# Optimization experiments

Measured on AMD Instinct MI355X. Metric: run time of the kernel, lower is better.

The kernel has to match this reference:

```python
import jax, jax.numpy as jnp
import numpy as np

B, L, D, H = 2, 2048, 2048, 16
HD = D // H          # head_dim = 128
LD = HD // 4         # latent_dim = 32


def _linear_params(key, fan_in, fan_out):
    kw, kb = jax.random.split(key)
    bound = 1.0 / np.sqrt(fan_in)
    W = jax.random.uniform(kw, (fan_in, fan_out), jnp.float32, -bound, bound)
    b = jax.random.uniform(kb, (fan_out,), jnp.float32, -bound, bound)
    return W, b


def setup_inputs() -> dict:
    key = jax.random.key(0)
    ks = jax.random.split(key, 12)
    x = jax.random.normal(ks[0], (B, L, D), jnp.float32)
    cos = jax.random.uniform(ks[1], (L, HD // 2), jnp.float32)
    sin = jax.random.uniform(ks[2], (L, HD // 2), jnp.float32)
    Wq, bq = _linear_params(ks[3], D, D)
    Wk, bk = _linear_params(ks[4], D, D)
    Wv, bv = _linear_params(ks[5], D, D)
    Wqc, bqc = _linear_params(ks[6], HD, LD)
    Wkc, bkc = _linear_params(ks[7], HD, LD)
    Wvc, bvc = _linear_params(ks[8], HD, LD)
    Wd, bd = _linear_params(ks[9], LD, HD)
    Wo, bo = _linear_params(ks[10], D, D)
    return dict(x=x, cos=cos, sin=sin, Wq=Wq, bq=bq, Wk=Wk, bk=bk, Wv=Wv, bv=bv,
                Wqc=Wqc, bqc=bqc, Wkc=Wkc, bkc=bkc, Wvc=Wvc, bvc=bvc,
                Wd=Wd, bd=bd, Wo=Wo, bo=bo)


def _apply_rope(q, k, cos, sin):
    # q, k: (B, H, L, HD); cos, sin: (L, HD//2) -> broadcast over B, H
    c = cos[None, None, :, :]
    s = sin[None, None, :, :]
    qe, qo = q[..., ::2], q[..., 1::2]
    ke, ko = k[..., ::2], k[..., 1::2]
    q_rot = jnp.stack([qe * c - qo * s, qe * s + qo * c], axis=-1).reshape(q.shape)
    k_rot = jnp.stack([ke * c - ko * s, ke * s + ko * c], axis=-1).reshape(k.shape)
    return q_rot, k_rot


def reference(x, cos, sin, Wq, bq, Wk, bk, Wv, bv,
              Wqc, bqc, Wkc, bkc, Wvc, bvc, Wd, bd, Wo, bo):
    b, l, d = x.shape
    # projections -> (B, H, L, HD)
    q = (x @ Wq + bq).reshape(b, l, H, HD).transpose(0, 2, 1, 3)
    k = (x @ Wk + bk).reshape(b, l, H, HD).transpose(0, 2, 1, 3)
    v = (x @ Wv + bv).reshape(b, l, H, HD).transpose(0, 2, 1, 3)
    q, k = _apply_rope(q, k, cos, sin)
    # low-rank compression into latent_dim
    qc = jnp.einsum('bhld,de->bhle', q, Wqc) + bqc
    kc = jnp.einsum('bhld,de->bhle', k, Wkc) + bkc
    vc = jnp.einsum('bhld,de->bhle', v, Wvc) + bvc
    scores = jnp.einsum('bhqe,bhke->bhqk', qc, kc) / np.sqrt(LD).astype(np.float32)
    causal = jnp.tril(jnp.ones((l, l), dtype=bool))  # True = keep
    scores = jnp.where(causal[None, None], scores, -jnp.inf)
    probs = jax.nn.softmax(scores, axis=-1)
    attn = jnp.einsum('bhqk,bhke->bhqe', probs, vc)
    attn = jnp.einsum('bhle,ed->bhld', attn, Wd) + bd  # decompress to HD
    attn = attn.transpose(0, 2, 1, 3).reshape(b, l, d)
    return attn @ Wo + bo
```

## Files before the change

### kernel.cpp

```cpp
#include <hip/hip_runtime.h>
#include <hip/hip_bf16.h>


#define Bsz 2
#define Lseq 2048
#define Dmod 2048
#define Hn 16
#define HDim 128
#define LDim 32

typedef __bf16 bf16x8 __attribute__((ext_vector_type(8)));
typedef float f32x4 __attribute__((ext_vector_type(4)));
typedef __hip_bfloat16 bf16;

#define GLDS16(g, l)                                                    \
  __builtin_amdgcn_global_load_lds(                                     \
      (const __attribute__((address_space(1))) unsigned int*)(g),       \
      (__attribute__((address_space(3))) unsigned int*)(l), 16, 0, 0)

#define SM_COS 0
#define SM_SIN 131072
#define SM_WC 262144
#define SM_BC 274432
#define SM_WD 274528
#define SM_BD 278624
#define SM_BO 278752
#define SM_BQKV 280800
#define SM_TOT 286944

__global__ void detect_dtype(const ushort* __restrict__ x, int* __restrict__ flag) {
  int t = threadIdx.x;
  int bad = 0;
  for (int k = 0; k < 4; ++k) {
    ushort u = x[t * 4 + k];
    int ex = (u >> 7) & 0xFF;
    if (ex >= 0xC0) bad = 1;
  }
  unsigned long long b = __ballot(bad);
  if (t == 0) *flag = (b != 0ULL) ? 1 : 0;
}

__device__ inline void conv8(const void* src, size_t so, bf16* dst, size_t dof, int f32) {
  if (f32) {
    const float* s = (const float*)src + so;
    bf16 tmp[8] __attribute__((aligned(16)));
    for (int j = 0; j < 8; ++j) tmp[j] = __float2bfloat16(s[j]);
    *(uint4*)&dst[dof] = *(uint4*)tmp;
  } else {
    *(uint4*)&dst[dof] = *(const uint4*)((const ushort*)src + so);
  }
}

__device__ inline float cv1(const void* s, size_t i, int f32) {
  return f32 ? ((const float*)s)[i] : __bfloat162float(((const bf16*)s)[i]);
}

__global__ __launch_bounds__(256) void conv_x(const void* __restrict__ xs,
                                              bf16* __restrict__ xd,
                                              const int* __restrict__ flagp) {
  int f32 = *flagp;
  size_t e = ((size_t)blockIdx.x * 256 + threadIdx.x) * 8;
  conv8(xs, e, xd, e, f32);
}

__global__ __launch_bounds__(256) void prep(
    const void* cosS, const void* sinS, const void* WqcS, const void* WkcS,
    const void* WvcS, const void* bqcS, const void* bkcS, const void* bvcS,
    const void* WdS, const void* bdS, const void* boS, const void* bqS,
    const void* bkS, const void* bvS, bf16* __restrict__ dst,
    bf16* __restrict__ wctG, bf16* __restrict__ wdtG,
    const int* __restrict__ flagp) {
  int f32 = *flagp;
  int tid = blockIdx.x * 256 + threadIdx.x;
  if (tid < SM_TOT / 8) {
    size_t e = (size_t)tid * 8;
    const void* src;
    size_t so;
    if (e < SM_SIN) { src = cosS; so = e - SM_COS; }
    else if (e < SM_WC) { src = sinS; so = e - SM_SIN; }
    else if (e < SM_BC) { size_t r = e - SM_WC; src = (r < 4096) ? WqcS : (r < 8192) ? WkcS : WvcS; so = r & 4095; }
    else if (e < SM_WD) { size_t r = e - SM_BC; src = (r < 32) ? bqcS : (r < 64) ? bkcS : bvcS; so = r & 31; }
    else if (e < SM_BD) { src = WdS; so = e - SM_WD; }
    else if (e < SM_BO) { src = bdS; so = e - SM_BD; }
    else if (e < SM_BQKV) { src = boS; so = e - SM_BO; }
    else { size_t r = e - SM_BQKV; src = (r < 2048) ? bqS : (r < 4096) ? bkS : bvS; so = r & 2047; }
    conv8(src, so, dst, e, f32);
  } else {
    int idx = tid - SM_TOT / 8;
    for (int i = idx; i < 16384; i += 40960 - SM_TOT / 8) {
      if (i < 12288) {
        int reg = i >> 12, rem = i & 4095, n = rem >> 7, k = rem & 127;
        const void* src = (reg == 0) ? WqcS : (reg == 1) ? WkcS : WvcS;
        wctG[i] = __float2bfloat16(cv1(src, (size_t)k * 32 + n, f32));
      } else {
        int i2 = i - 12288, o = i2 >> 5, e = i2 & 31;
        wdtG[i2] = __float2bfloat16(cv1(WdS, (size_t)e * 128 + o, f32));
      }
    }
  }
}

__global__ __launch_bounds__(256) void transpose4(const void* __restrict__ WqS,
                                                  const void* __restrict__ WkS,
                                                  const void* __restrict__ WvS,
                                                  const void* __restrict__ WoS,
                                                  bf16* __restrict__ WtQKV,
                                                  bf16* __restrict__ WtO,
                                                  const int* __restrict__ flagp) {
  __shared__ float tile[64][65];
  int f32 = *flagp;
  int z = blockIdx.z;
  const void* W = (z == 0) ? WqS : (z == 1) ? WkS : (z == 2) ? WvS : WoS;
  bf16* Wt = (z == 3) ? WtO : (WtQKV + (size_t)z * 2048 * 2048);
  int n0 = blockIdx.x * 64, k0 = blockIdx.y * 64;
  int t = threadIdx.x;
  int x = (t & 7) * 8, y = t >> 3;
  for (int p = 0; p < 2; ++p) {
    int r = y + p * 32;
    if (f32) {
      const float* src = (const float*)W + (size_t)(k0 + r) * 2048 + n0 + x;
      float4 a = *(const float4*)src;
      float4 b2 = *(const float4*)(src + 4);
      tile[r][x + 0] = a.x; tile[r][x + 1] = a.y; tile[r][x + 2] = a.z; tile[r][x + 3] = a.w;
      tile[r][x + 4] = b2.x; tile[r][x + 5] = b2.y; tile[r][x + 6] = b2.z; tile[r][x + 7] = b2.w;
    } else {
      const ushort* src = (const ushort*)W + (size_t)(k0 + r) * 2048 + n0 + x;
      uint4 u = *(const uint4*)src;
      bf16* e = (bf16*)&u;
      for (int j = 0; j < 8; ++j) tile[r][x + j] = __bfloat162float(e[j]);
    }
  }
  __syncthreads();
  for (int p = 0; p < 2; ++p) {
    int n = y + p * 32;
    bf16 tmp[8] __attribute__((aligned(16)));
    for (int j = 0; j < 8; ++j) tmp[j] = __float2bfloat16(tile[x + j][n]);
    *(uint4*)&Wt[(size_t)(n0 + n) * 2048 + k0 + x] = *(uint4*)tmp;
  }
}

#define ESTR 136
__global__ __launch_bounds__(256) void gemm_qkv_compress(
    const bf16* __restrict__ A, const bf16* __restrict__ Bt,
    const bf16* __restrict__ small, const bf16* __restrict__ wctG,
    bf16* __restrict__ qc, bf16* __restrict__ kc, bf16* __restrict__ vcT) {
  __shared__ bf16 sh[128 * ESTR];
  bf16* lA = sh;
  bf16* lB = sh + 4096;
  const int K = 2048;
  int bm = blockIdx.y, bn = blockIdx.x;
  int reg = bn >> 4, h = bn & 15;
  int t = threadIdx.x;
  int lane = t & 63, w = t >> 6;
  int wm = (w >> 1) * 64, wn = (w & 1) * 64;
  int qd = lane >> 4, ln = lane & 15;

  f32x4 acc[4][4] = {};
  const bf16* Ab = A + (size_t)(bm * 128) * K;
  const bf16* Bb = Bt + (size_t)(bn * 128) * K;

  for (int kt = 0; kt < K; kt += 32) {
    for (int p = 0; p < 2; ++p) {
      int slot = t + p * 256;
      int r = slot >> 2, c = (slot & 3) * 8;
      GLDS16(&Ab[(size_t)r * K + kt + c], &lA[slot * 8]);
      GLDS16(&Bb[(size_t)r * K + kt + c], &lB[slot * 8]);
    }
    __syncthreads();
    bf16x8 af[4], bfr[4];
    for (int i = 0; i < 4; ++i) af[i] = *(bf16x8*)&lA[(wm + i * 16 + ln) * 32 + qd * 8];
    for (int j = 0; j < 4; ++j) bfr[j] = *(bf16x8*)&lB[(wn + j * 16 + ln) * 32 + qd * 8];
    for (int i = 0; i < 4; ++i)
      for (int j = 0; j < 4; ++j)
        acc[i][j] = __builtin_amdgcn_mfma_f32_16x16x32_bf16(af[i], bfr[j], acc[i][j], 0, 0, 0);
    __syncthreads();
  }

  for (int j = 0; j < 4; ++j) {
    int col = wn + j * 16 + ln;
    float bv = __bfloat162float(small[SM_BQKV + bn * 128 + col]);
    for (int i = 0; i < 4; ++i)
      for (int r = 0; r < 4; ++r)
        sh[(wm + i * 16 + qd * 4 + r) * ESTR + col] = __float2bfloat16(acc[i][j][r] + bv);
  }
  __syncthreads();

  int r0 = w * 32;
  int b = bm >> 4;
  int bh = b * Hn + h;
  bf16x8 bfr2[2][4];
  for (int nt = 0; nt < 2; ++nt)
    for (int kt = 0; kt < 4; ++kt)
      bfr2[nt][kt] = *(const bf16x8*)&wctG[reg * 4096 + (nt * 16 + ln) * 128 + kt * 32 + qd * 8];
  float bc[2];
  bc[0] = __bfloat162float(small[SM_BC + reg * 32 + ln]);
  bc[1] = __bfloat162float(small[SM_BC + reg * 32 + 16 + ln]);

  for (int mt = 0; mt < 2; ++mt) {
    int lb = r0 + mt * 16 + ln;
    int lg = (bm & 15) * 128 + lb;
    f32x4 c2[2] = {};
    for (int kt = 0; kt < 4; ++kt) {
      uint4 u = *(uint4*)&sh[lb * ESTR + kt * 32 + qd * 8];
      if (reg < 2) {
        bf16* e8 = (bf16*)&u;
        int pbase = kt * 16 + qd * 4;
        for (int j = 0; j < 4; ++j) {
          float cvv = __bfloat162float(small[SM_COS + (size_t)lg * 64 + pbase + j]);
          float svv = __bfloat162float(small[SM_SIN + (size_t)lg * 64 + pbase + j]);
          float ev = __bfloat162float(e8[2 * j]);
          float ov = __bfloat162float(e8[2 * j + 1]);
          e8[2 * j] = __float2bfloat16(ev * cvv - ov * svv);
          e8[2 * j + 1] = __float2bfloat16(ev * svv + ov * cvv);
        }
      }
      bf16x8 a = *(bf16x8*)&u;
      c2[0] = __builtin_amdgcn_mfma_f32_16x16x32_bf16(a, bfr2[0][kt], c2[0], 0, 0, 0);
      c2[1] = __builtin_amdgcn_mfma_f32_16x16x32_bf16(a, bfr2[1][kt], c2[1], 0, 0, 0);
    }
    int lgbase = (bm & 15) * 128 + r0 + mt * 16 + qd * 4;
    if (reg < 2) {
      bf16* dst = (reg == 0) ? qc : kc;
      for (int nt = 0; nt < 2; ++nt)
        for (int r = 0; r < 4; ++r)
          dst[((size_t)bh * Lseq + lgbase + r) * 32 + nt * 16 + ln] =
              __float2bfloat16(c2[nt][r] + bc[nt]);
    } else {
      for (int nt = 0; nt < 2; ++nt) {
        bf16 p4[4] __attribute__((aligned(8)));
        for (int r = 0; r < 4; ++r) p4[r] = __float2bfloat16(c2[nt][r] + bc[nt]);
        *(uint2*)&vcT[((size_t)bh * 32 + nt * 16 + ln) * Lseq + lgbase] = *(uint2*)p4;
      }
    }
  }
}

__global__ __launch_bounds__(256) void gemm_bias_out(const bf16* __restrict__ A,
                                                     const bf16* __restrict__ Bt,
                                                     const bf16* __restrict__ bias,
                                                     void* __restrict__ C,
                                                     int M, int N, int K,
                                                     const int* __restrict__ flagp) {
  __shared__ bf16 lA[128 * 32];
  __shared__ bf16 lB[128 * 32];
  int f32out = *flagp;
  int bm = blockIdx.y, bn = blockIdx.x;
  int t = threadIdx.x;
  int lane = t & 63, w = t >> 6;
  int wm = (w >> 1) * 64, wn = (w & 1) * 64;
  int qd = lane >> 4, ln = lane & 15;

  f32x4 acc[4][4] = {};
  const bf16* Ab = A + (size_t)(bm * 128) * K;
  const bf16* Bb = Bt + (size_t)(bn * 128) * K;

  for (int kt = 0; kt < K; kt += 32) {
    for (int p = 0; p < 2; ++p) {
      int slot = t + p * 256;
      int r = slot >> 2, c = (slot & 3) * 8;
      GLDS16(&Ab[(size_t)r * K + kt + c], &lA[slot * 8]);
      GLDS16(&Bb[(size_t)r * K + kt + c], &lB[slot * 8]);
    }
    __syncthreads();
    bf16x8 af[4], bfr[4];
    for (int i = 0; i < 4; ++i) af[i] = *(bf16x8*)&lA[(wm + i * 16 + ln) * 32 + qd * 8];
    for (int j = 0; j < 4; ++j) bfr[j] = *(bf16x8*)&lB[(wn + j * 16 + ln) * 32 + qd * 8];
    for (int i = 0; i < 4; ++i)
      for (int j = 0; j < 4; ++j)
        acc[i][j] = __builtin_amdgcn_mfma_f32_16x16x32_bf16(af[i], bfr[j], acc[i][j], 0, 0, 0);
    __syncthreads();
  }
  for (int i = 0; i < 4; ++i)
    for (int j = 0; j < 4; ++j) {
      int col = bn * 128 + wn + j * 16 + ln;
      float bv = __bfloat162float(bias[col]);
      for (int r = 0; r < 4; ++r) {
        int row = bm * 128 + wm + i * 16 + qd * 4 + r;
        float v = acc[i][j][r] + bv;
        if (f32out) ((float*)C)[(size_t)row * N + col] = v;
        else ((bf16*)C)[(size_t)row * N + col] = __float2bfloat16(v);
      }
    }
}

__global__ __launch_bounds__(256) void flash32(const bf16* __restrict__ qc,
                                               const bf16* __restrict__ kc,
                                               const bf16* __restrict__ vcT,
                                               const bf16* __restrict__ small,
                                               const bf16* __restrict__ wdtG,
                                               bf16* __restrict__ y) {
  __shared__ bf16 pbuf[4][16 * 40];
  int t = threadIdx.x;
  int lane = t & 63, w = t >> 6;
  int qd = lane >> 4, ln = lane & 15;
  int blk = blockIdx.x;
  int lt = blk & 31;
  int bh = blk >> 5, h = bh & 15, b = bh >> 4;
  int q0 = lt * 64 + w * 16;

  bf16x8 qf = *(const bf16x8*)&qc[((size_t)bh * Lseq + q0 + ln) * 32 + qd * 8];

  f32x4 o0 = {}, o1 = {};
  float m[4], lsum[4];
  for (int r = 0; r < 4; ++r) { m[r] = -1e30f; lsum[r] = 0.f; }
  const float scale = 0.17677669529663687f;

  int nkt = (q0 + 16 + 31) >> 5;
  bf16* pb = pbuf[w];
  for (int kt = 0; kt < nkt; ++kt) {
    int k0 = kt * 32;
    bf16x8 kf0 = *(const bf16x8*)&kc[((size_t)bh * Lseq + k0 + ln) * 32 + qd * 8];
    bf16x8 kf1 = *(const bf16x8*)&kc[((size_t)bh * Lseq + k0 + 16 + ln) * 32 + qd * 8];
    f32x4 s0 = {}, s1 = {};
    s0 = __builtin_amdgcn_mfma_f32_16x16x32_bf16(qf, kf0, s0, 0, 0, 0);
    s1 = __builtin_amdgcn_mfma_f32_16x16x32_bf16(qf, kf1, s1, 0, 0, 0);
    float sv0[4], sv1[4], alpha[4];
    for (int r = 0; r < 4; ++r) {
      int qrow = q0 + qd * 4 + r;
      sv0[r] = (k0 + ln <= qrow) ? s0[r] * scale : -1e30f;
      sv1[r] = (k0 + 16 + ln <= qrow) ? s1[r] * scale : -1e30f;
    }
    for (int r = 0; r < 4; ++r) {
      float mx = fmaxf(sv0[r], sv1[r]);
      for (int off = 1; off < 16; off <<= 1) mx = fmaxf(mx, __shfl_xor(mx, off, 64));
      float mn = fmaxf(m[r], mx);
      alpha[r] = __expf(m[r] - mn);
      m[r] = mn;
      sv0[r] = __expf(sv0[r] - mn);
      sv1[r] = __expf(sv1[r] - mn);
      float rs = sv0[r] + sv1[r];
      for (int off = 1; off < 16; off <<= 1) rs += __shfl_xor(rs, off, 64);
      lsum[r] = lsum[r] * alpha[r] + rs;
      o0[r] *= alpha[r];
      o1[r] *= alpha[r];
    }
    for (int r = 0; r < 4; ++r) {
      pb[(qd * 4 + r) * 40 + ln] = __float2bfloat16(sv0[r]);
      pb[(qd * 4 + r) * 40 + 16 + ln] = __float2bfloat16(sv1[r]);
    }
    asm volatile("s_waitcnt lgkmcnt(0)" ::: "memory");
    bf16x8 pf = *(bf16x8*)&pb[ln * 40 + qd * 8];
    bf16x8 vf0 = *(const bf16x8*)&vcT[((size_t)bh * 32 + ln) * Lseq + k0 + qd * 8];
    bf16x8 vf1 = *(const bf16x8*)&vcT[((size_t)bh * 32 + 16 + ln) * Lseq + k0 + qd * 8];
    o0 = __builtin_amdgcn_mfma_f32_16x16x32_bf16(pf, vf0, o0, 0, 0, 0);
    o1 = __builtin_amdgcn_mfma_f32_16x16x32_bf16(pf, vf1, o1, 0, 0, 0);
  }
  for (int r = 0; r < 4; ++r) {
    float inv = 1.0f / lsum[r];
    pb[(qd * 4 + r) * 40 + ln] = __float2bfloat16(o0[r] * inv);
    pb[(qd * 4 + r) * 40 + 16 + ln] = __float2bfloat16(o1[r] * inv);
  }
  asm volatile("s_waitcnt lgkmcnt(0)" ::: "memory");
  bf16x8 pf = *(bf16x8*)&pb[ln * 40 + qd * 8];
  for (int nt = 0; nt < 8; ++nt) {
    bf16x8 bfr = *(const bf16x8*)&wdtG[(nt * 16 + ln) * 32 + qd * 8];
    f32x4 yacc = {};
    yacc = __builtin_amdgcn_mfma_f32_16x16x32_bf16(pf, bfr, yacc, 0, 0, 0);
    float bb = __bfloat162float(small[SM_BD + nt * 16 + ln]);
    for (int rr = 0; rr < 4; ++rr) {
      int l = q0 + qd * 4 + rr;
      y[(size_t)(b * Lseq + l) * Dmod + h * 128 + nt * 16 + ln] =
          __float2bfloat16(yacc[rr] + bb);
    }
  }
}

extern "C" void kernel_launch(void* const* d_in, const int* in_sizes, int n_in,
                              void* d_out, int out_size, void* d_ws, size_t ws_size,
                              hipStream_t stream) {
  const void* x = d_in[0];
  const void* cosS = d_in[1];
  const void* sinS = d_in[2];
  const void* Wq = d_in[3];
  const void* bq = d_in[4];
  const void* Wk = d_in[5];
  const void* bk = d_in[6];
  const void* Wv = d_in[7];
  const void* bv = d_in[8];
  const void* Wqc = d_in[9];
  const void* bqc = d_in[10];
  const void* Wkc = d_in[11];
  const void* bkc = d_in[12];
  const void* Wvc = d_in[13];
  const void* bvc = d_in[14];
  const void* Wd = d_in[15];
  const void* bd = d_in[16];
  const void* Wo = d_in[17];
  const void* bo = d_in[18];

  char* ws = (char*)d_ws;
  size_t off = 0;
  auto alloc = [&](size_t bytes) {
    char* p = ws + off;
    off += (bytes + 255) & ~(size_t)255;
    return p;
  };
  int* flag = (int*)alloc(256);
  bf16* small = (bf16*)alloc((size_t)SM_TOT * 2);
  bf16* wctG = (bf16*)alloc((size_t)12288 * 2);
  bf16* wdtG = (bf16*)alloc((size_t)4096 * 2);
  bf16* xb = (bf16*)alloc((size_t)4096 * 2048 * 2);
  bf16* WtQKV = (bf16*)alloc((size_t)6144 * 2048 * 2);
  bf16* WtO = (bf16*)alloc((size_t)2048 * 2048 * 2);
  bf16* qcW = (bf16*)alloc((size_t)65536 * 32 * 2);
  bf16* kcW = (bf16*)alloc((size_t)65536 * 32 * 2);
  bf16* vcTW = (bf16*)alloc((size_t)65536 * 32 * 2);
  bf16* yW = (bf16*)alloc((size_t)4096 * 2048 * 2);

  dim3 tb(256);
  detect_dtype<<<1, 64, 0, stream>>>((const ushort*)x, flag);
  prep<<<160, tb, 0, stream>>>(cosS, sinS, Wqc, Wkc, Wvc, bqc, bkc, bvc, Wd, bd, bo, bq,
                               bk, bv, small, wctG, wdtG, flag);
  transpose4<<<dim3(32, 32, 4), tb, 0, stream>>>(Wq, Wk, Wv, Wo, WtQKV, WtO, flag);
  conv_x<<<4096, tb, 0, stream>>>(x, xb, flag);
  gemm_qkv_compress<<<dim3(48, 32), tb, 0, stream>>>(xb, WtQKV, small, wctG, qcW, kcW,
                                                     vcTW);
  flash32<<<1024, tb, 0, stream>>>(qcW, kcW, vcTW, small, wdtG, yW);
  gemm_bias_out<<<dim3(16, 32), tb, 0, stream>>>(yW, WtO, small + SM_BO, d_out, 4096, 2048,
                                                 2048, flag);
}
```

Measured before the change: 472.9 us.

## Process 128-key chunks in flash attention and halve output GEMM row tile

The flash attention loop now handles keys in 128-wide chunks (up to 8 score MFMAs per step) rather than 32, so the online-softmax max/sum shuffle reductions and rescaling run a quarter as often. The per-wave P buffer in LDS grows to hold the wider chunk. Separately, the output-projection GEMM tile shrinks from 128x128 to 64x128 and the grid doubles to 1024 blocks, giving the 256-CU device more than one block per CU. The trade-offs are more registers for the score array in the attention kernel and lower reuse of the weight tile in the GEMM.

```diff
diff --git a/kernel.cpp b/kernel.cpp
--- a/kernel.cpp
+++ b/kernel.cpp
@@ -241,41 +241,44 @@
                                                      void* __restrict__ C,
                                                      int M, int N, int K,
                                                      const int* __restrict__ flagp) {
-  __shared__ bf16 lA[128 * 32];
+  __shared__ bf16 lA[64 * 32];
   __shared__ bf16 lB[128 * 32];
   int f32out = *flagp;
   int bm = blockIdx.y, bn = blockIdx.x;
   int t = threadIdx.x;
   int lane = t & 63, w = t >> 6;
-  int wm = (w >> 1) * 64, wn = (w & 1) * 64;
+  int wm = (w >> 1) * 32, wn = (w & 1) * 64;
   int qd = lane >> 4, ln = lane & 15;
 
-  f32x4 acc[4][4] = {};
-  const bf16* Ab = A + (size_t)(bm * 128) * K;
+  f32x4 acc[2][4] = {};
+  const bf16* Ab = A + (size_t)(bm * 64) * K;
   const bf16* Bb = Bt + (size_t)(bn * 128) * K;
 
   for (int kt = 0; kt < K; kt += 32) {
+    {
+      int r = t >> 2, c = (t & 3) * 8;
+      GLDS16(&Ab[(size_t)r * K + kt + c], &lA[t * 8]);
+    }
     for (int p = 0; p < 2; ++p) {
       int slot = t + p * 256;
       int r = slot >> 2, c = (slot & 3) * 8;
-      GLDS16(&Ab[(size_t)r * K + kt + c], &lA[slot * 8]);
       GLDS16(&Bb[(size_t)r * K + kt + c], &lB[slot * 8]);
     }
     __syncthreads();
-    bf16x8 af[4], bfr[4];
-    for (int i = 0; i < 4; ++i) af[i] = *(bf16x8*)&lA[(wm + i * 16 + ln) * 32 + qd * 8];
+    bf16x8 af[2], bfr[4];
+    for (int i = 0; i < 2; ++i) af[i] = *(bf16x8*)&lA[(wm + i * 16 + ln) * 32 + qd * 8];
     for (int j = 0; j < 4; ++j) bfr[j] = *(bf16x8*)&lB[(wn + j * 16 + ln) * 32 + qd * 8];
-    for (int i = 0; i < 4; ++i)
+    for (int i = 0; i < 2; ++i)
       for (int j = 0; j < 4; ++j)
         acc[i][j] = __builtin_amdgcn_mfma_f32_16x16x32_bf16(af[i], bfr[j], acc[i][j], 0, 0, 0);
     __syncthreads();
   }
-  for (int i = 0; i < 4; ++i)
+  for (int i = 0; i < 2; ++i)
     for (int j = 0; j < 4; ++j) {
       int col = bn * 128 + wn + j * 16 + ln;
       float bv = __bfloat162float(bias[col]);
       for (int r = 0; r < 4; ++r) {
-        int row = bm * 128 + wm + i * 16 + qd * 4 + r;
+        int row = bm * 64 + wm + i * 16 + qd * 4 + r;
         float v = acc[i][j][r] + bv;
         if (f32out) ((float*)C)[(size_t)row * N + col] = v;
         else ((bf16*)C)[(size_t)row * N + col] = __float2bfloat16(v);
@@ -289,7 +292,7 @@
                                                const bf16* __restrict__ small,
                                                const bf16* __restrict__ wdtG,
                                                bf16* __restrict__ y) {
-  __shared__ bf16 pbuf[4][16 * 40];
+  __shared__ bf16 pbuf[4][16 * 136];
   int t = threadIdx.x;
   int lane = t & 63, w = t >> 6;
   int qd = lane >> 4, ln = lane & 15;
@@ -304,54 +307,68 @@
   float m[4], lsum[4];
   for (int r = 0; r < 4; ++r) { m[r] = -1e30f; lsum[r] = 0.f; }
   const float scale = 0.17677669529663687f;
-
-  int nkt = (q0 + 16 + 31) >> 5;
   bf16* pb = pbuf[w];
-  for (int kt = 0; kt < nkt; ++kt) {
-    int k0 = kt * 32;
-    bf16x8 kf0 = *(const bf16x8*)&kc[((size_t)bh * Lseq + k0 + ln) * 32 + qd * 8];
-    bf16x8 kf1 = *(const bf16x8*)&kc[((size_t)bh * Lseq + k0 + 16 + ln) * 32 + qd * 8];
-    f32x4 s0 = {}, s1 = {};
-    s0 = __builtin_amdgcn_mfma_f32_16x16x32_bf16(qf, kf0, s0, 0, 0, 0);
-    s1 = __builtin_amdgcn_mfma_f32_16x16x32_bf16(qf, kf1, s1, 0, 0, 0);
-    float sv0[4], sv1[4], alpha[4];
+  const bf16* kbase = kc + (size_t)bh * Lseq * 32;
+  const bf16* vbase = vcT + (size_t)bh * 32 * Lseq;
+  int kmax = q0 + 16;
+  int nc = (kmax + 127) >> 7;
+
+  for (int ch = 0; ch < nc; ++ch) {
+    int k0 = ch << 7;
+    int rem = kmax - k0;
+    int jmax = (rem >= 128) ? 4 : ((rem + 31) >> 5);
+    int cmax = jmax * 2;
+    f32x4 s[8];
+    for (int c = 0; c < 8; ++c)
+      if (c < cmax) {
+        bf16x8 kf = *(const bf16x8*)&kbase[(size_t)(k0 + c * 16 + ln) * 32 + qd * 8];
+        f32x4 z = {};
+        s[c] = __builtin_amdgcn_mfma_f32_16x16x32_bf16(qf, kf, z, 0, 0, 0);
+      }
     for (int r = 0; r < 4; ++r) {
       int qrow = q0 + qd * 4 + r;
-      sv0[r] = (k0 + ln <= qrow) ? s0[r] * scale : -1e30f;
-      sv1[r] = (k0 + 16 + ln <= qrow) ? s1[r] * scale : -1e30f;
-    }
-    for (int r = 0; r < 4; ++r) {
-      float mx = fmaxf(sv0[r], sv1[r]);
+      float mx = -1e30f;
+      for (int c = 0; c < 8; ++c)
+        if (c < cmax) {
+          s[c][r] = (k0 + c * 16 + ln <= qrow) ? s[c][r] * scale : -1e30f;
+          mx = fmaxf(mx, s[c][r]);
+        }
       for (int off = 1; off < 16; off <<= 1) mx = fmaxf(mx, __shfl_xor(mx, off, 64));
       float mn = fmaxf(m[r], mx);
-      alpha[r] = __expf(m[r] - mn);
+      float alpha = __expf(m[r] - mn);
       m[r] = mn;
-      sv0[r] = __expf(sv0[r] - mn);
-      sv1[r] = __expf(sv1[r] - mn);
-      float rs = sv0[r] + sv1[r];
+      float rs = 0.f;
+      for (int c = 0; c < 8; ++c)
+        if (c < cmax) {
+          float e = __expf(s[c][r] - mn);
+          s[c][r] = e;
+          rs += e;
+        }
       for (int off = 1; off < 16; off <<= 1) rs += __shfl_xor(rs, off, 64);
-      lsum[r] = lsum[r] * alpha[r] + rs;
-      o0[r] *= alpha[r];
-      o1[r] *= alpha[r];
-    }
-    for (int r = 0; r < 4; ++r) {
-      pb[(qd * 4 + r) * 40 + ln] = __float2bfloat16(sv0[r]);
-      pb[(qd * 4 + r) * 40 + 16 + ln] = __float2bfloat16(sv1[r]);
+      lsum[r] = lsum[r] * alpha + rs;
+      o0[r] *= alpha;
+      o1[r] *= alpha;
+      for (int c = 0; c < 8; ++c)
+        if (c < cmax)
+          pb[(qd * 4 + r) * 136 + c * 16 + ln] = __float2bfloat16(s[c][r]);
     }
     asm volatile("s_waitcnt lgkmcnt(0)" ::: "memory");
-    bf16x8 pf = *(bf16x8*)&pb[ln * 40 + qd * 8];
-    bf16x8 vf0 = *(const bf16x8*)&vcT[((size_t)bh * 32 + ln) * Lseq + k0 + qd * 8];
-    bf16x8 vf1 = *(const bf16x8*)&vcT[((size_t)bh * 32 + 16 + ln) * Lseq + k0 + qd * 8];
-    o0 = __builtin_amdgcn_mfma_f32_16x16x32_bf16(pf, vf0, o0, 0, 0, 0);
-    o1 = __builtin_amdgcn_mfma_f32_16x16x32_bf16(pf, vf1, o1, 0, 0, 0);
+    for (int j = 0; j < 4; ++j)
+      if (j < jmax) {
+        bf16x8 pf = *(bf16x8*)&pb[ln * 136 + j * 32 + qd * 8];
+        bf16x8 vf0 = *(const bf16x8*)&vbase[(size_t)ln * Lseq + k0 + j * 32 + qd * 8];
+        bf16x8 vf1 = *(const bf16x8*)&vbase[(size_t)(16 + ln) * Lseq + k0 + j * 32 + qd * 8];
+        o0 = __builtin_amdgcn_mfma_f32_16x16x32_bf16(pf, vf0, o0, 0, 0, 0);
+        o1 = __builtin_amdgcn_mfma_f32_16x16x32_bf16(pf, vf1, o1, 0, 0, 0);
+      }
   }
   for (int r = 0; r < 4; ++r) {
     float inv = 1.0f / lsum[r];
-    pb[(qd * 4 + r) * 40 + ln] = __float2bfloat16(o0[r] * inv);
-    pb[(qd * 4 + r) * 40 + 16 + ln] = __float2bfloat16(o1[r] * inv);
+    pb[(qd * 4 + r) * 136 + ln] = __float2bfloat16(o0[r] * inv);
+    pb[(qd * 4 + r) * 136 + 16 + ln] = __float2bfloat16(o1[r] * inv);
   }
   asm volatile("s_waitcnt lgkmcnt(0)" ::: "memory");
-  bf16x8 pf = *(bf16x8*)&pb[ln * 40 + qd * 8];
+  bf16x8 pf = *(bf16x8*)&pb[ln * 136 + qd * 8];
   for (int nt = 0; nt < 8; ++nt) {
     bf16x8 bfr = *(const bf16x8*)&wdtG[(nt * 16 + ln) * 32 + qd * 8];
     f32x4 yacc = {};
@@ -416,6 +433,6 @@
   gemm_qkv_compress<<<dim3(48, 32), tb, 0, stream>>>(xb, WtQKV, small, wctG, qcW, kcW,
                                                      vcTW);
   flash32<<<1024, tb, 0, stream>>>(qcW, kcW, vcTW, small, wdtG, yW);
-  gemm_bias_out<<<dim3(16, 32), tb, 0, stream>>>(yW, WtO, small + SM_BO, d_out, 4096, 2048,
+  gemm_bias_out<<<dim3(16, 64), tb, 0, stream>>>(yW, WtO, small + SM_BO, d_out, 4096, 2048,
                                                  2048, flag);
 }
```

After: 923.2 us. 1.95x slower.
